# Kernel optimization log

Hardware: AMD Instinct MI355X
Metric: run time of the kernel (lower is better)

The kernel has to match this reference:

```python
import jax, jax.numpy as jnp
import numpy as np

H = 8          # num_heads
BM = 128       # block_size_m
BN = 128       # block_size_n
EPS = 1e-6
CAUSAL = True  # config.causal


def setup_inputs() -> dict:
    key = jax.random.key(0)
    ks = jax.random.split(key, 5)
    B, N, D = 1, 2048, 512
    s = 1.0 / np.sqrt(D)
    # small-scale x so projected points mostly stay inside the Poincare ball
    x = jax.random.normal(ks[0], (B, N, D), jnp.float32) * 0.05
    return {
        'x': x,
        'c': jnp.ones((1,), jnp.float32),
        'Wq': jax.random.normal(ks[1], (D, D), jnp.float32) * s,
        'bq': jnp.zeros((D,), jnp.float32),
        'Wk': jax.random.normal(ks[2], (D, D), jnp.float32) * s,
        'bk': jnp.zeros((D,), jnp.float32),
        'Wv': jax.random.normal(ks[3], (D, D), jnp.float32) * s,
        'bv': jnp.zeros((D,), jnp.float32),
        'Wo': jax.random.normal(ks[4], (D, D), jnp.float32) * s,
        'bo': jnp.zeros((D,), jnp.float32),
    }


def reference(x, c, Wq, bq, Wk, bk, Wv, bv, Wo, bo):
    B, N, D = x.shape
    Dh = D // H
    cc = jnp.clip(jnp.abs(c), 1e-6)            # (1,) learned curvature, abs+clamp as in torch
    sqrt_c = jnp.sqrt(jnp.clip(cc, EPS))

    def proj(W, b):
        return (x @ W + b).reshape(B, N, H, Dh).transpose(0, 2, 1, 3)  # (B,H,N,Dh)

    q, k, v = proj(Wq, bq), proj(Wk, bk), proj(Wv, bv)

    # Poincare distance: ||q-k||^2 expanded via norms (same math as explicit diff tensor)
    qn = (q ** 2).sum(-1)                      # (B,H,N)
    kn = (k ** 2).sum(-1)                      # (B,H,N)
    qk = jnp.einsum('bhmd,bhnd->bhmn', q, k)   # (B,H,N,N)
    diff_sq = jnp.clip(qn[..., :, None] + kn[..., None, :] - 2.0 * qk, 0.0)
    denom = jnp.clip((1.0 - cc * qn)[..., :, None] * (1.0 - cc * kn)[..., None, :], EPS)
    arg = jnp.clip(1.0 + 2.0 * cc * diff_sq / denom, 1.0 + EPS)
    scores = -jnp.arccosh(arg) / sqrt_c        # (B,H,N,N)

    # block-wise softmax: each 128x128 block subtracts ITS OWN max (faithful to torch code,
    # which omits cross-block max rescaling), then exp-sums are accumulated across blocks.
    nbm, nbn = N // BM, N // BN
    s = scores.reshape(B, H, nbm, BM, nbn, BN)
    row = jnp.arange(nbm)[:, None]
    col = jnp.arange(nbn)[None, :]
    skip = (col > row) if CAUSAL else jnp.zeros((nbm, nbn), bool)   # skipped upper blocks
    diag = (col == row) if CAUSAL else jnp.zeros((nbm, nbn), bool)
    tri = jnp.triu(jnp.ones((BM, BN), bool), 1)
    mask = skip[:, None, :, None] | (diag[:, None, :, None] & tri[None, :, None, :])  # (nbm,BM,nbn,BN)

    s_masked = jnp.where(mask, -jnp.inf, s)
    bmax = s_masked.max(axis=-1, keepdims=True)                      # per-block-row max over BN
    bmax = jnp.where(jnp.isfinite(bmax), bmax, 0.0)                  # skipped blocks -> safe
    e = jnp.where(mask, 0.0, jnp.exp(s - bmax))                      # (B,H,nbm,BM,nbn,BN)

    normalizer = jnp.clip(e.sum(axis=(4, 5)).reshape(B, H, N), EPS)  # (B,H,N)
    vb = v.reshape(B, H, nbn, BN, Dh)
    out = jnp.einsum('bhrmcn,bhcnd->bhrmd', e, vb).reshape(B, H, N, Dh)
    out = out / normalizer[..., None]
    out = out.transpose(0, 2, 1, 3).reshape(B, N, D)
    return out @ Wo + bo
```

## Files before the change

kernel.cpp:

```cpp
#include <hip/hip_runtime.h>
#include <math.h>

#define D_MODEL 512
#define NHEADS  8
#define NSEQ    2048
#define NBLK    16
#define NCHUNK  72
#define EPSF    1e-6f
#define WPLANE  262144

typedef _Float16 v8h __attribute__((ext_vector_type(8)));
typedef _Float16 v4h __attribute__((ext_vector_type(4)));
typedef float    v4f __attribute__((ext_vector_type(4)));

static __device__ __forceinline__ v4f mfma16h(v8h a, v8h b, v4f c) {
  return __builtin_amdgcn_mfma_f32_16x16x32_f16(a, b, c, 0, 0, 0);
}

#define GLLDS(gp, lp)                                                          \
  __builtin_amdgcn_global_load_lds(                                            \
      (const __attribute__((address_space(1))) unsigned int*)(const void*)(gp),\
      (__attribute__((address_space(3))) unsigned int*)(void*)(lp), 16, 0, 0)

__global__ __launch_bounds__(256) void prep_wx(const float* __restrict__ W0,
                                               const float* __restrict__ W1,
                                               const float* __restrict__ W2,
                                               const float* __restrict__ W3,
                                               const float* __restrict__ x,
                                               _Float16* __restrict__ Wth,
                                               _Float16* __restrict__ xh) {
  const int z = blockIdx.z;
  const int tid = threadIdx.x;
  if (z == 4) {
    const int wg = blockIdx.y * 8 + blockIdx.x;
    int base = wg * 4096 + tid;
#pragma unroll
    for (int l = 0; l < 16; ++l) {
      int idx = base + l * 256;
      float4 v = reinterpret_cast<const float4*>(x)[idx];
      v4h o;
      o[0] = (_Float16)v.x; o[1] = (_Float16)v.y;
      o[2] = (_Float16)v.z; o[3] = (_Float16)v.w;
      reinterpret_cast<v4h*>(xh)[idx] = o;
    }
    return;
  }
  __shared__ float T[64][68];
  const float* W = (z == 0) ? W0 : (z == 1) ? W1 : (z == 2) ? W2 : W3;
  const int kb = blockIdx.x * 64;
  const int nb = blockIdx.y * 64;
#pragma unroll
  for (int l = 0; l < 4; ++l) {
    int f = tid + l * 256;
    int row = f >> 4, c4 = f & 15;
    float4 v = *reinterpret_cast<const float4*>(&W[(size_t)(kb + row) * D_MODEL + nb + c4 * 4]);
    T[c4 * 4 + 0][row] = v.x; T[c4 * 4 + 1][row] = v.y;
    T[c4 * 4 + 2][row] = v.z; T[c4 * 4 + 3][row] = v.w;
  }
  __syncthreads();
  _Float16* oh = Wth + (size_t)z * WPLANE;
#pragma unroll
  for (int l = 0; l < 4; ++l) {
    int f = tid + l * 256;
    int n_ = f >> 4, k4 = f & 15;
    v4h h4;
    h4[0] = (_Float16)T[n_][k4 * 4 + 0];
    h4[1] = (_Float16)T[n_][k4 * 4 + 1];
    h4[2] = (_Float16)T[n_][k4 * 4 + 2];
    h4[3] = (_Float16)T[n_][k4 * 4 + 3];
    *reinterpret_cast<v4h*>(&oh[(size_t)(nb + n_) * D_MODEL + kb + k4 * 4]) = h4;
  }
}

__global__ __launch_bounds__(256) void qkv_gemm(
    const _Float16* __restrict__ xh, const _Float16* __restrict__ Wth,
    const float* __restrict__ bq, const float* __restrict__ bk,
    const float* __restrict__ bv,
    _Float16* __restrict__ Qp, _Float16* __restrict__ Kp,
    _Float16* __restrict__ Vtb,
    float* __restrict__ Qn_, float* __restrict__ Kn_) {
  __shared__ _Float16 Ah[64][72];
  __shared__ _Float16 Bh[64][72];
  __shared__ float npar[2][64];
  const int z = blockIdx.z;
  const _Float16* Bt = Wth + (size_t)z * WPLANE;
  const float* bias = (z == 0) ? bq : (z == 1) ? bk : bv;
  _Float16* outp = (z == 0) ? Qp : Kp;

  const int bx = blockIdx.x, by = blockIdx.y;
  const int tid = threadIdx.x;
  const int wid = tid >> 6, lane = tid & 63;
  const int wr = wid >> 1, wc = wid & 1;
  const int g = lane >> 4, lx = lane & 15;

  v4f acc[2][2];
#pragma unroll
  for (int i = 0; i < 2; ++i)
#pragma unroll
    for (int j = 0; j < 2; ++j) acc[i][j] = v4f{0.f, 0.f, 0.f, 0.f};

  for (int k0 = 0; k0 < 8; ++k0) {
    __syncthreads();
#pragma unroll
    for (int l = 0; l < 2; ++l) {
      int f = tid + l * 256;
      int row = f >> 3, c8 = f & 7;
      *reinterpret_cast<uint4*>(&Ah[row][c8 * 8]) =
          *reinterpret_cast<const uint4*>(&xh[(size_t)(by * 64 + row) * D_MODEL + k0 * 64 + c8 * 8]);
      *reinterpret_cast<uint4*>(&Bh[row][c8 * 8]) =
          *reinterpret_cast<const uint4*>(&Bt[(size_t)(bx * 64 + row) * D_MODEL + k0 * 64 + c8 * 8]);
    }
    __syncthreads();
    v8h a[2][2], b[2][2];
#pragma unroll
    for (int i = 0; i < 2; ++i)
#pragma unroll
      for (int ks = 0; ks < 2; ++ks) {
        a[i][ks] = *reinterpret_cast<const v8h*>(&Ah[wr * 32 + i * 16 + lx][ks * 32 + g * 8]);
        b[i][ks] = *reinterpret_cast<const v8h*>(&Bh[wc * 32 + i * 16 + lx][ks * 32 + g * 8]);
      }
#pragma unroll
    for (int i = 0; i < 2; ++i)
#pragma unroll
      for (int j = 0; j < 2; ++j) {
        acc[i][j] = mfma16h(a[i][0], b[j][0], acc[i][j]);
        acc[i][j] = mfma16h(a[i][1], b[j][1], acc[i][j]);
      }
  }

  if (z < 2) {
    float np[2][4];
#pragma unroll
    for (int i = 0; i < 2; ++i)
#pragma unroll
      for (int r = 0; r < 4; ++r) np[i][r] = 0.f;
#pragma unroll
    for (int j = 0; j < 2; ++j) {
      const int col = bx * 64 + wc * 32 + j * 16 + lx;
      const float bj = bias[col];
#pragma unroll
      for (int i = 0; i < 2; ++i)
#pragma unroll
        for (int r = 0; r < 4; ++r) {
          const int row = by * 64 + wr * 32 + i * 16 + g * 4 + r;
          float v = acc[i][j][r] + bj;
          _Float16 hv = (_Float16)v;
          outp[(size_t)row * D_MODEL + col] = hv;
          float vr = (float)hv;
          np[i][r] = fmaf(vr, vr, np[i][r]);
        }
    }
#pragma unroll
    for (int i = 0; i < 2; ++i)
#pragma unroll
      for (int r = 0; r < 4; ++r) {
        float s = np[i][r];
        s += __shfl_xor(s, 1, 64);
        s += __shfl_xor(s, 2, 64);
        s += __shfl_xor(s, 4, 64);
        s += __shfl_xor(s, 8, 64);
        if (lx == 0) npar[wc][wr * 32 + i * 16 + g * 4 + r] = s;
      }
    __syncthreads();
    if (tid < 64) {
      float s = npar[0][tid] + npar[1][tid];
      float* Nout = (z == 0) ? Qn_ : Kn_;
      Nout[bx * NSEQ + by * 64 + tid] = s;
    }
  } else {
    __syncthreads();
    _Float16* Tv = &Ah[0][0];
#pragma unroll
    for (int j = 0; j < 2; ++j) {
      const int col = wc * 32 + j * 16 + lx;
      const float bj = bias[bx * 64 + col];
#pragma unroll
      for (int i = 0; i < 2; ++i)
#pragma unroll
        for (int r = 0; r < 4; ++r) {
          const int row = wr * 32 + i * 16 + g * 4 + r;
          Tv[row * 72 + col] = (_Float16)(acc[i][j][r] + bj);
        }
    }
    __syncthreads();
#pragma unroll
    for (int l = 0; l < 2; ++l) {
      int f = tid + l * 256;
      int d = f >> 3, ch = f & 7;
      ushort tmp[8];
#pragma unroll
      for (int jj = 0; jj < 8; ++jj)
        tmp[jj] = ((const ushort*)Tv)[(ch * 8 + jj) * 72 + d];
      *reinterpret_cast<uint4*>(&Vtb[(size_t)(bx * 64 + d) * NSEQ + by * 64 + ch * 8]) =
          *reinterpret_cast<const uint4*>(tmp);
    }
  }
}

__global__ __launch_bounds__(512, 4) void attn(
    const _Float16* __restrict__ Qp, const _Float16* __restrict__ Kp,
    const _Float16* __restrict__ Vtb, const float* __restrict__ Qn,
    const float* __restrict__ Kn, const float* __restrict__ cptr,
    _Float16* __restrict__ Opart, float* __restrict__ Npart)
{
  __shared__ _Float16 KhsF[8192];
  __shared__ _Float16 VsF[8192];
  __shared__ _Float16 Es[8][16][68];
  __shared__ float kns2[256];

  const int bid = blockIdx.x;
  const int h    = bid & 7;
  const int pid2 = bid >> 3;
  int m = 0, base = 0;
  while (base + (m / 2 + 1) <= pid2) { base += m / 2 + 1; ++m; }
  const int c  = pid2 - base;
  const int n0 = 2 * c;
  const int n1 = (n0 + 1 < m) ? n0 + 1 : m;
  const bool two = (n1 != n0);

  const int tid  = threadIdx.x;
  const int w    = tid >> 6;
  const int lane = tid & 63;
  const int g = lane >> 4, lx = lane & 15;

  const float cc = fmaxf(fabsf(cptr[0]), 1e-6f);
  const float is = rsqrtf(cc);
  const bool is_one = (cc == 1.0f);
  const float two_cc = 2.f * cc;

  const _Float16* Kgh = Kp + h * 64;
  const _Float16* Vgh = Vtb + (size_t)(h * 64) * NSEQ;

  const int krow0 = tid >> 3;
  const int klc   = (tid & 7) ^ (krow0 & 7);
  const int vd0   = tid >> 4;
  const int vlc   = (tid & 15) ^ (vd0 & 7);

#define ISSUE_K(nn)                                                           \
  do {                                                                        \
    GLLDS(&Kgh[(size_t)((nn) * 128 + krow0) * D_MODEL + klc * 8],             \
          &KhsF[w * 512]);                                                    \
    GLLDS(&Kgh[(size_t)((nn) * 128 + krow0 + 64) * D_MODEL + klc * 8],        \
          &KhsF[4096 + w * 512]);                                             \
  } while (0)
#define ISSUE_V(nn)                                                           \
  do {                                                                        \
    GLLDS(&Vgh[(size_t)vd0 * NSEQ + (nn) * 128 + vlc * 8],                    \
          &VsF[w * 512]);                                                     \
    GLLDS(&Vgh[(size_t)(vd0 + 32) * NSEQ + (nn) * 128 + vlc * 8],             \
          &VsF[4096 + w * 512]);                                              \
  } while (0)

  ISSUE_K(n0);
  ISSUE_V(n0);
  if (tid < 128) kns2[tid] = Kn[h * NSEQ + n0 * 128 + tid];
  else if (two && tid < 256) kns2[tid] = Kn[h * NSEQ + n1 * 128 + (tid - 128)];

  v8h aQ[2];
  {
    const size_t qoff = (size_t)(m * 128 + 16 * w + lx) * D_MODEL + h * 64 + g * 8;
    aQ[0] = *reinterpret_cast<const v8h*>(&Qp[qoff]);
    aQ[1] = *reinterpret_cast<const v8h*>(&Qp[qoff + 32]);
  }
  float qnr[4], qar[4];
#pragma unroll
  for (int r = 0; r < 4; ++r) {
    qnr[r] = Qn[h * NSEQ + m * 128 + 16 * w + g * 4 + r];
    qar[r] = fmaf(-cc, qnr[r], 1.f);
  }

  v4f o_acc[4];
#pragma unroll
  for (int td = 0; td < 4; ++td) o_acc[td] = v4f{0.f, 0.f, 0.f, 0.f};
  float nrm[4] = {0.f, 0.f, 0.f, 0.f};

  __syncthreads();

  v4f acc[8];
  const int swz = lx & 7;

#pragma unroll
  for (int tn = 0; tn < 8; ++tn) {
    const int rb = (tn * 16 + lx) * 64;
    v8h b0 = *reinterpret_cast<const v8h*>(&KhsF[rb + ((g ^ swz) * 8)]);
    v8h b1 = *reinterpret_cast<const v8h*>(&KhsF[rb + (((g ^ swz) ^ 4) * 8)]);
    v4f a = v4f{0.f, 0.f, 0.f, 0.f};
    a = mfma16h(aQ[0], b0, a);
    a = mfma16h(aQ[1], b1, a);
    acc[tn] = a;
  }
  if (two) {
    __syncthreads();
    ISSUE_K(n1);
  }

#pragma unroll
  for (int it = 0; it < 2; ++it) {
    if (it == 1 && !two) break;
    const int n = (it == 0) ? n0 : n1;
    const int kofs = it * 128;

    if (it == 1) {
#pragma unroll
      for (int tn = 0; tn < 8; ++tn) {
        const int rb = (tn * 16 + lx) * 64;
        v8h b0 = *reinterpret_cast<const v8h*>(&KhsF[rb + ((g ^ swz) * 8)]);
        v8h b1 = *reinterpret_cast<const v8h*>(&KhsF[rb + (((g ^ swz) ^ 4) * 8)]);
        v4f a = v4f{0.f, 0.f, 0.f, 0.f};
        a = mfma16h(aQ[0], b0, a);
        a = mfma16h(aQ[1], b1, a);
        acc[tn] = a;
      }
    }

    const bool diag = (n == m);
#pragma unroll
    for (int tn = 0; tn < 8; ++tn) {
      const int col = tn * 16 + lx;
      const float knc = kns2[kofs + col];
      const float kac = fmaf(-cc, knc, 1.f);
#pragma unroll
      for (int r = 0; r < 4; ++r) {
        const int rowl = 16 * w + g * 4 + r;
        float dsq = fmaxf(fmaf(-2.f, acc[tn][r], qnr[r] + knc), 0.f);
        float den = fmaxf(qar[r] * kac, EPSF);
        float t = fmaxf(two_cc * dsq * __builtin_amdgcn_rcpf(den), EPSF);
        float u = 1.f + t + __builtin_amdgcn_sqrtf(t * (t + 2.f));
        if (diag && col > rowl) u = __builtin_inff();
        acc[tn][r] = u;
      }
    }

    float mred[4];
    if (is_one) {
#pragma unroll
      for (int r = 0; r < 4; ++r) mred[r] = __builtin_inff();
#pragma unroll
      for (int tn = 0; tn < 8; ++tn)
#pragma unroll
        for (int r = 0; r < 4; ++r) mred[r] = fminf(mred[r], acc[tn][r]);
#pragma unroll
      for (int d = 1; d < 16; d <<= 1)
#pragma unroll
        for (int r = 0; r < 4; ++r) mred[r] = fminf(mred[r], __shfl_xor(mred[r], d, 64));
    } else {
#pragma unroll
      for (int r = 0; r < 4; ++r) mred[r] = -__builtin_inff();
#pragma unroll
      for (int tn = 0; tn < 8; ++tn)
#pragma unroll
        for (int r = 0; r < 4; ++r) {
          float s = -__logf(acc[tn][r]) * is;
          acc[tn][r] = s;
          mred[r] = fmaxf(mred[r], s);
        }
#pragma unroll
      for (int d = 1; d < 16; d <<= 1)
#pragma unroll
        for (int r = 0; r < 4; ++r) mred[r] = fmaxf(mred[r], __shfl_xor(mred[r], d, 64));
    }

#pragma unroll
    for (int half = 0; half < 2; ++half) {
#pragma unroll
      for (int tn2 = 0; tn2 < 4; ++tn2) {
        const int tn = half * 4 + tn2;
#pragma unroll
        for (int r = 0; r < 4; ++r) {
          float e = is_one ? mred[r] * __builtin_amdgcn_rcpf(acc[tn][r])
                           : __expf(acc[tn][r] - mred[r]);
          nrm[r] += e;
          Es[w][g * 4 + r][tn2 * 16 + lx] = (_Float16)e;
        }
      }
      if (it == 1 && half == 0) {
        asm volatile("s_waitcnt vmcnt(0) lgkmcnt(0)" ::: "memory");
      } else {
        asm volatile("s_waitcnt lgkmcnt(0)" ::: "memory");
      }
      __builtin_amdgcn_sched_barrier(0);
#pragma unroll
      for (int ks2 = 0; ks2 < 2; ++ks2) {
        const int ks = half * 2 + ks2;
        v8h ea = *reinterpret_cast<const v8h*>(&Es[w][lx][ks2 * 32 + g * 8]);
#pragma unroll
        for (int td = 0; td < 4; ++td) {
          v8h vb = *reinterpret_cast<const v8h*>(
              &VsF[(td * 16 + lx) * 128 + (((ks * 4 + g) ^ swz) * 8)]);
          o_acc[td] = mfma16h(ea, vb, o_acc[td]);
        }
      }
    }

    if (it == 0 && two) {
      __syncthreads();
      ISSUE_V(n1);
    }
  }

#pragma unroll
  for (int d = 1; d < 16; d <<= 1)
#pragma unroll
    for (int r = 0; r < 4; ++r) nrm[r] += __shfl_xor(nrm[r], d, 64);

  _Float16* Op = Opart + ((size_t)h * NCHUNK + pid2) * 8192;
#pragma unroll
  for (int td = 0; td < 4; ++td)
#pragma unroll
    for (int r = 0; r < 4; ++r)
      Op[(size_t)(((w * 4 + td) * 4) + r) * 64 + lane] = (_Float16)o_acc[td][r];

  {
    const int sel = lane & 3;
    float tmp = (sel == 0) ? nrm[0] : (sel == 1) ? nrm[1] : (sel == 2) ? nrm[2] : nrm[3];
    const int src = ((lane >> 2) & 3) * 16 + (lane & 3);
    float nval = __shfl(tmp, src, 64);
    if (lane < 16)
      Npart[((size_t)h * NCHUNK + pid2) * 128 + 16 * w + lane] = nval;
  }
#undef ISSUE_K
#undef ISSUE_V
}

__global__ __launch_bounds__(256) void reduce_o(const _Float16* __restrict__ Opart,
                                                const float* __restrict__ Npart,
                                                _Float16* __restrict__ Of) {
  const int mq = blockIdx.x;
  const int mm = mq >> 2;
  const int rq = (mq & 3) * 32;
  const int h  = blockIdx.y;
  const int tid = threadIdx.x;
  int base = 0;
  for (int k = 0; k < mm; ++k) base += k / 2 + 1;
  const int nch = mm / 2 + 1;

  __shared__ float T[32][68];
  __shared__ float innorm[32];
  if (tid < 32) {
    float s = 0.f;
    for (int cI = 0; cI < nch; ++cI)
      s += Npart[((size_t)h * NCHUNK + base + cI) * 128 + rq + tid];
    innorm[tid] = 1.f / fmaxf(s, EPSF);
  }
  const int wbase = rq >> 4;
#pragma unroll
  for (int l = 0; l < 8; ++l) {
    int idx = tid + l * 256;
    int lane = idx & 63;
    int sub  = idx >> 6;
    int r = sub & 3, td = (sub >> 2) & 3, wloc = sub >> 4;
    int w = wbase + wloc;
    const size_t off = (size_t)((w * 4 + td) * 4 + r) * 64 + lane;
    float s = 0.f;
    for (int cI = 0; cI < nch; ++cI)
      s += (float)Opart[((size_t)h * NCHUNK + base + cI) * 8192 + off];
    int row = 16 * wloc + 4 * (lane >> 4) + r;
    int col = td * 16 + (lane & 15);
    T[row][col] = s;
  }
  __syncthreads();
#pragma unroll
  for (int l = 0; l < 2; ++l) {
    int f = tid + l * 256;
    int row = f >> 4, c4 = f & 15;
    float inv = innorm[row];
    v4h o4;
    o4[0] = (_Float16)(T[row][c4 * 4 + 0] * inv);
    o4[1] = (_Float16)(T[row][c4 * 4 + 1] * inv);
    o4[2] = (_Float16)(T[row][c4 * 4 + 2] * inv);
    o4[3] = (_Float16)(T[row][c4 * 4 + 3] * inv);
    *reinterpret_cast<v4h*>(
        &Of[(size_t)(mm * 128 + rq + row) * D_MODEL + h * 64 + c4 * 4]) = o4;
  }
}

__global__ __launch_bounds__(256) void o_gemm(const _Float16* __restrict__ Of,
                                              const _Float16* __restrict__ Wth,
                                              const float* __restrict__ bo,
                                              float* __restrict__ out) {
  __shared__ _Float16 As[64][40], Bs[64][40];
  const _Float16* Bt = Wth + (size_t)3 * WPLANE;
  const int bx = blockIdx.x, by = blockIdx.y;
  const int tid = threadIdx.x;
  const int wid = tid >> 6, lane = tid & 63;
  const int wr = wid >> 1, wc = wid & 1;
  const int g = lane >> 4, lx = lane & 15;

  v4f acc[2][2];
#pragma unroll
  for (int i = 0; i < 2; ++i)
#pragma unroll
    for (int j = 0; j < 2; ++j) acc[i][j] = v4f{0.f, 0.f, 0.f, 0.f};

  const int srow = tid >> 2, sc8 = tid & 3;
  for (int k0 = 0; k0 < 16; ++k0) {
    __syncthreads();
    *reinterpret_cast<uint4*>(&As[srow][sc8 * 8]) =
        *reinterpret_cast<const uint4*>(&Of[(size_t)(by * 64 + srow) * D_MODEL + k0 * 32 + sc8 * 8]);
    *reinterpret_cast<uint4*>(&Bs[srow][sc8 * 8]) =
        *reinterpret_cast<const uint4*>(&Bt[(size_t)(bx * 64 + srow) * D_MODEL + k0 * 32 + sc8 * 8]);
    __syncthreads();
    v8h ah[2], bh[2];
#pragma unroll
    for (int i = 0; i < 2; ++i) {
      ah[i] = *reinterpret_cast<const v8h*>(&As[wr * 32 + i * 16 + lx][g * 8]);
      bh[i] = *reinterpret_cast<const v8h*>(&Bs[wc * 32 + i * 16 + lx][g * 8]);
    }
#pragma unroll
    for (int i = 0; i < 2; ++i)
#pragma unroll
      for (int j = 0; j < 2; ++j)
        acc[i][j] = mfma16h(ah[i], bh[j], acc[i][j]);
  }
#pragma unroll
  for (int j = 0; j < 2; ++j) {
    const int col = bx * 64 + wc * 32 + j * 16 + lx;
    const float bj = bo[col];
#pragma unroll
    for (int i = 0; i < 2; ++i)
#pragma unroll
      for (int r = 0; r < 4; ++r) {
        const int row = by * 64 + wr * 32 + i * 16 + g * 4 + r;
        out[(size_t)row * D_MODEL + col] = acc[i][j][r] + bj;
      }
  }
}

extern "C" void kernel_launch(void* const* d_in, const int* in_sizes, int n_in,
                              void* d_out, int out_size, void* d_ws, size_t ws_size,
                              hipStream_t stream) {
  (void)in_sizes; (void)n_in; (void)out_size; (void)ws_size;
  const float* x  = (const float*)d_in[0];
  const float* cfg= (const float*)d_in[1];
  const float* Wq = (const float*)d_in[2];
  const float* bq = (const float*)d_in[3];
  const float* Wk = (const float*)d_in[4];
  const float* bk = (const float*)d_in[5];
  const float* Wv = (const float*)d_in[6];
  const float* bv = (const float*)d_in[7];
  const float* Wo = (const float*)d_in[8];
  const float* bo = (const float*)d_in[9];
  float* out = (float*)d_out;

  char* p = (char*)d_ws;
  const size_t PL = (size_t)NSEQ * D_MODEL * sizeof(_Float16);
  _Float16* Wth = (_Float16*)p;        p += 4 * (size_t)WPLANE * sizeof(_Float16);
  _Float16* xhp = (_Float16*)p;        p += PL;
  _Float16* Qp  = (_Float16*)p;        p += PL;
  _Float16* Kp  = (_Float16*)p;        p += PL;
  _Float16* Vtb = (_Float16*)p;        p += PL;
  _Float16* Of  = (_Float16*)p;        p += PL;
  float*  Qn  = (float*)p;             p += (size_t)NHEADS * NSEQ * sizeof(float);
  float*  Kn  = (float*)p;             p += (size_t)NHEADS * NSEQ * sizeof(float);
  _Float16* Opart = (_Float16*)p;      p += (size_t)NHEADS * NCHUNK * 8192 * sizeof(_Float16);
  float*  Npart = (float*)p;

  prep_wx<<<dim3(8, 8, 5), 256, 0, stream>>>(Wq, Wk, Wv, Wo, x, Wth, xhp);
  qkv_gemm<<<dim3(8, 32, 3), 256, 0, stream>>>(xhp, Wth, bq, bk, bv,
                                               Qp, Kp, Vtb, Qn, Kn);
  attn<<<dim3(NCHUNK * NHEADS), 512, 0, stream>>>(Qp, Kp, Vtb, Qn, Kn, cfg,
                                                  Opart, Npart);
  reduce_o<<<dim3(64, NHEADS), 256, 0, stream>>>(Opart, Npart, Of);
  o_gemm<<<dim3(8, 32), 256, 0, stream>>>(Of, Wth, bo, out);
}
```

Before: 78.37 us.

## Fuse split-K reduction into attention via last-block atomic counter

Removes the separate reduce_o kernel launch. Each attention block increments a per-(head, row-block) atomic counter, and the last block to finish sums the partial outputs and normalizers, then writes the normalized fp16 output directly. The counters are zeroed inside prep_wx. This saves one launch and its dependency gap, at the cost of a serialized tail reduction done by a single block per row-block, plus extra threadfences and atomics.

```diff
diff --git a/kernel.cpp b/kernel.cpp
--- a/kernel.cpp
+++ b/kernel.cpp
@@ -28,11 +28,13 @@
                                                const float* __restrict__ W3,
                                                const float* __restrict__ x,
                                                _Float16* __restrict__ Wth,
-                                               _Float16* __restrict__ xh) {
+                                               _Float16* __restrict__ xh,
+                                               int* __restrict__ cnt) {
   const int z = blockIdx.z;
   const int tid = threadIdx.x;
   if (z == 4) {
     const int wg = blockIdx.y * 8 + blockIdx.x;
+    if (wg == 0 && tid < NBLK * NHEADS) cnt[tid] = 0;
     int base = wg * 4096 + tid;
 #pragma unroll
     for (int l = 0; l < 16; ++l) {
@@ -201,12 +203,15 @@
     const _Float16* __restrict__ Qp, const _Float16* __restrict__ Kp,
     const _Float16* __restrict__ Vtb, const float* __restrict__ Qn,
     const float* __restrict__ Kn, const float* __restrict__ cptr,
-    _Float16* __restrict__ Opart, float* __restrict__ Npart)
+    _Float16* __restrict__ Opart, float* __restrict__ Npart,
+    _Float16* __restrict__ Of, int* __restrict__ cnt)
 {
   __shared__ _Float16 KhsF[8192];
   __shared__ _Float16 VsF[8192];
   __shared__ _Float16 Es[8][16][68];
   __shared__ float kns2[256];
+  __shared__ float innorm[128];
+  __shared__ int lastflag;
 
   const int bid = blockIdx.x;
   const int h    = bid & 7;
@@ -418,60 +423,60 @@
     if (lane < 16)
       Npart[((size_t)h * NCHUNK + pid2) * 128 + 16 * w + lane] = nval;
   }
+
+  const int nch = m / 2 + 1;
+  __syncthreads();
+  if (tid == 0) {
+    __threadfence();
+    int old = __hip_atomic_fetch_add(&cnt[h * NBLK + m], 1,
+                                     __ATOMIC_ACQ_REL, __HIP_MEMORY_SCOPE_AGENT);
+    lastflag = (old == nch - 1);
+  }
+  __syncthreads();
+  if (!lastflag) return;
+  __threadfence();
+
+  const size_t pbase = (size_t)h * NCHUNK + base;
+  if (tid < 128) {
+    float s = 0.f;
+    for (int cI = 0; cI < nch; ++cI)
+      s += Npart[(pbase + cI) * 128 + tid];
+    innorm[tid] = 1.f / fmaxf(s, EPSF);
+  }
+  __syncthreads();
+  {
+    const int e0  = tid * 16;
+    const int sub = e0 >> 6;
+    const int ln0 = e0 & 63;
+    float s[16];
+#pragma unroll
+    for (int jj = 0; jj < 16; ++jj) s[jj] = 0.f;
+    for (int cI = 0; cI < nch; ++cI) {
+      const _Float16* src = Opart + (pbase + cI) * 8192 + sub * 64 + ln0;
+      v8h a = *reinterpret_cast<const v8h*>(src);
+      v8h b = *reinterpret_cast<const v8h*>(src + 8);
+#pragma unroll
+      for (int jj = 0; jj < 8; ++jj) {
+        s[jj]     += (float)a[jj];
+        s[8 + jj] += (float)b[jj];
+      }
+    }
+    const int wq = sub >> 4, td = (sub >> 2) & 3, rr = sub & 3;
+    const int gq = ln0 >> 4;
+    const int row = 16 * wq + 4 * gq + rr;
+    const float inv = innorm[row];
+    _Float16* dst = &Of[(size_t)(m * 128 + row) * D_MODEL + h * 64 + td * 16];
+    v8h o0, o1;
+#pragma unroll
+    for (int jj = 0; jj < 8; ++jj) {
+      o0[jj] = (_Float16)(s[jj] * inv);
+      o1[jj] = (_Float16)(s[8 + jj] * inv);
+    }
+    *reinterpret_cast<v8h*>(dst)     = o0;
+    *reinterpret_cast<v8h*>(dst + 8) = o1;
+  }
 #undef ISSUE_K
 #undef ISSUE_V
-}
-
-__global__ __launch_bounds__(256) void reduce_o(const _Float16* __restrict__ Opart,
-                                                const float* __restrict__ Npart,
-                                                _Float16* __restrict__ Of) {
-  const int mq = blockIdx.x;
-  const int mm = mq >> 2;
-  const int rq = (mq & 3) * 32;
-  const int h  = blockIdx.y;
-  const int tid = threadIdx.x;
-  int base = 0;
-  for (int k = 0; k < mm; ++k) base += k / 2 + 1;
-  const int nch = mm / 2 + 1;
-
-  __shared__ float T[32][68];
-  __shared__ float innorm[32];
-  if (tid < 32) {
-    float s = 0.f;
-    for (int cI = 0; cI < nch; ++cI)
-      s += Npart[((size_t)h * NCHUNK + base + cI) * 128 + rq + tid];
-    innorm[tid] = 1.f / fmaxf(s, EPSF);
-  }
-  const int wbase = rq >> 4;
-#pragma unroll
-  for (int l = 0; l < 8; ++l) {
-    int idx = tid + l * 256;
-    int lane = idx & 63;
-    int sub  = idx >> 6;
-    int r = sub & 3, td = (sub >> 2) & 3, wloc = sub >> 4;
-    int w = wbase + wloc;
-    const size_t off = (size_t)((w * 4 + td) * 4 + r) * 64 + lane;
-    float s = 0.f;
-    for (int cI = 0; cI < nch; ++cI)
-      s += (float)Opart[((size_t)h * NCHUNK + base + cI) * 8192 + off];
-    int row = 16 * wloc + 4 * (lane >> 4) + r;
-    int col = td * 16 + (lane & 15);
-    T[row][col] = s;
-  }
-  __syncthreads();
-#pragma unroll
-  for (int l = 0; l < 2; ++l) {
-    int f = tid + l * 256;
-    int row = f >> 4, c4 = f & 15;
-    float inv = innorm[row];
-    v4h o4;
-    o4[0] = (_Float16)(T[row][c4 * 4 + 0] * inv);
-    o4[1] = (_Float16)(T[row][c4 * 4 + 1] * inv);
-    o4[2] = (_Float16)(T[row][c4 * 4 + 2] * inv);
-    o4[3] = (_Float16)(T[row][c4 * 4 + 3] * inv);
-    *reinterpret_cast<v4h*>(
-        &Of[(size_t)(mm * 128 + rq + row) * D_MODEL + h * 64 + c4 * 4]) = o4;
-  }
 }
 
 __global__ __launch_bounds__(256) void o_gemm(const _Float16* __restrict__ Of,
@@ -553,13 +558,13 @@
   float*  Qn  = (float*)p;             p += (size_t)NHEADS * NSEQ * sizeof(float);
   float*  Kn  = (float*)p;             p += (size_t)NHEADS * NSEQ * sizeof(float);
   _Float16* Opart = (_Float16*)p;      p += (size_t)NHEADS * NCHUNK * 8192 * sizeof(_Float16);
-  float*  Npart = (float*)p;
-
-  prep_wx<<<dim3(8, 8, 5), 256, 0, stream>>>(Wq, Wk, Wv, Wo, x, Wth, xhp);
+  float*  Npart = (float*)p;           p += (size_t)NHEADS * NCHUNK * 128 * sizeof(float);
+  int*    cnt   = (int*)p;
+
+  prep_wx<<<dim3(8, 8, 5), 256, 0, stream>>>(Wq, Wk, Wv, Wo, x, Wth, xhp, cnt);
   qkv_gemm<<<dim3(8, 32, 3), 256, 0, stream>>>(xhp, Wth, bq, bk, bv,
                                                Qp, Kp, Vtb, Qn, Kn);
   attn<<<dim3(NCHUNK * NHEADS), 512, 0, stream>>>(Qp, Kp, Vtb, Qn, Kn, cfg,
-                                                  Opart, Npart);
-  reduce_o<<<dim3(64, NHEADS), 256, 0, stream>>>(Opart, Npart, Of);
+                                                  Opart, Npart, Of, cnt);
   o_gemm<<<dim3(8, 32), 256, 0, stream>>>(Of, Wth, bo, out);
 }
```

New measurement: 96.01 us. 22.5% more time.
